# Kernel tuning notes

Hardware: AMD Instinct MI355X
Metric: run time of the kernel (lower is better)

The kernel has to match this reference:

```python
import jax, jax.numpy as jnp
import numpy as np

D_MODEL = 384
D_INNER = 768   # expand=2
D_STATE = 16
DT_RANK = 24    # ceil(d_model/16)
D_CONV = 4
VOCAB = 50257
AUDIO_DIM = 80
B, L_AUDIO, L_TEXT = 2, 1024, 1024


def _conv1d(x, w, b, pad_l, pad_r, groups=1):
    # x: [B, C, L], w: [O, I/groups, K]
    y = jax.lax.conv_general_dilated(
        x, w, window_strides=(1,), padding=[(pad_l, pad_r)],
        feature_group_count=groups, dimension_numbers=('NCH', 'OIH', 'NCH'))
    return y + b[None, :, None]


def _mamba(x, in_w, convw, convb, xproj_w, dt_w, dt_b, A_log, Dp, out_w):
    # x: [B, L, D_MODEL]
    Bn, L, _ = x.shape
    xz = x @ in_w.T                       # [B, L, 2*D_INNER]
    xi, z = jnp.split(xz, 2, axis=-1)
    # causal depthwise conv (torch pads d_conv-1 both sides then slices [:L])
    xi = _conv1d(xi.transpose(0, 2, 1), convw, convb, D_CONV - 1, 0, groups=D_INNER)
    xi = jax.nn.silu(xi.transpose(0, 2, 1))          # [B, L, D_INNER]
    xdbl = xi @ xproj_w.T                            # [B, L, DT_RANK+2*D_STATE]
    dt, Bm, Cm = jnp.split(xdbl, [DT_RANK, DT_RANK + D_STATE], axis=-1)
    dt = jax.nn.softplus(dt @ dt_w.T + dt_b)         # [B, L, D_INNER]
    A = -jnp.exp(A_log)                              # [D_INNER, D_STATE]
    dA = jnp.exp(dt[..., None] * A)                  # [B, L, D_INNER, D_STATE]
    dBu = dt[..., None] * Bm[:, :, None, :] * xi[..., None]

    def step(h, inputs):
        dA_t, dBu_t, C_t = inputs
        h = dA_t * h + dBu_t                         # [B, D_INNER, D_STATE]
        y = jnp.einsum('bdn,bn->bd', h, C_t)
        return h, y

    h0 = jnp.zeros((Bn, D_INNER, D_STATE), dtype=x.dtype)
    _, ys = jax.lax.scan(step, h0,
                         (dA.transpose(1, 0, 2, 3), dBu.transpose(1, 0, 2, 3), Cm.transpose(1, 0, 2)))
    y = ys.transpose(1, 0, 2) + xi * Dp              # D skip connection
    y = y * jax.nn.silu(z)                           # gate
    return y @ out_w.T                               # [B, L, D_MODEL]


def setup_inputs() -> dict:
    key = jax.random.key(0)
    ks = jax.random.split(key, 16)

    def rn(k, shape, s=0.02):
        return jax.random.normal(k, shape, jnp.float32) * s

    inp = {}
    inp['audio_features'] = jax.random.normal(ks[0], (B, AUDIO_DIM, L_AUDIO), jnp.float32)
    inp['text_tokens'] = jax.random.randint(ks[1], (B, L_TEXT), 0, VOCAB)
    inp['conv1_w'] = rn(ks[2], (D_MODEL // 2, AUDIO_DIM, 3))
    inp['conv1_b'] = jnp.zeros((D_MODEL // 2,), jnp.float32)
    inp['conv2_w'] = rn(ks[3], (D_MODEL, D_MODEL // 2, 3))
    inp['conv2_b'] = jnp.zeros((D_MODEL,), jnp.float32)
    inp['embed'] = rn(ks[4], (VOCAB, D_MODEL))

    def mamba_params(kbase):
        kk = jax.random.split(kbase, 6)
        A = jnp.tile(jnp.arange(1, D_STATE + 1, dtype=jnp.float32), (D_INNER, 1))
        return dict(in_w=rn(kk[0], (2 * D_INNER, D_MODEL)),
                    convw=rn(kk[1], (D_INNER, 1, D_CONV)),
                    convb=jnp.zeros((D_INNER,), jnp.float32),
                    xproj_w=rn(kk[2], (DT_RANK + 2 * D_STATE, D_INNER)),
                    dt_w=rn(kk[3], (D_INNER, DT_RANK)),
                    dt_b=rn(kk[4], (D_INNER,), 0.1),
                    A_log=jnp.log(A),
                    Dp=jnp.ones((D_INNER,), jnp.float32),
                    out_w=rn(kk[5], (D_MODEL, D_INNER)))

    for i, p in enumerate([mamba_params(ks[5]), mamba_params(ks[6])], 1):
        for n, v in p.items():
            inp[f'm{i}_{n}'] = v
    inp['proj_w'] = rn(ks[7], (VOCAB, D_MODEL))
    inp['proj_b'] = jnp.zeros((VOCAB,), jnp.float32)
    return inp


def reference(audio_features, text_tokens, conv1_w, conv1_b, conv2_w, conv2_b, embed,
              m1_in_w, m1_convw, m1_convb, m1_xproj_w, m1_dt_w, m1_dt_b, m1_A_log, m1_Dp, m1_out_w,
              m2_in_w, m2_convw, m2_convb, m2_xproj_w, m2_dt_w, m2_dt_b, m2_A_log, m2_Dp, m2_out_w,
              proj_w, proj_b):
    a = jax.nn.relu(_conv1d(audio_features, conv1_w, conv1_b, 1, 1))
    a = _conv1d(a, conv2_w, conv2_b, 1, 1)
    audio_emb = a.transpose(0, 2, 1)                 # [B, L_audio, D_MODEL]
    text_emb = embed[text_tokens]                    # [B, L_text, D_MODEL]
    x = jnp.concatenate([audio_emb, text_emb], axis=1)
    x = _mamba(x, m1_in_w, m1_convw, m1_convb, m1_xproj_w, m1_dt_w, m1_dt_b, m1_A_log, m1_Dp, m1_out_w)
    x = _mamba(x, m2_in_w, m2_convw, m2_convb, m2_xproj_w, m2_dt_w, m2_dt_b, m2_A_log, m2_Dp, m2_out_w)
    return x @ proj_w.T + proj_b                     # [B, L, VOCAB]
```

## Files before the change

kernel.cpp:

```cpp
#include <hip/hip_runtime.h>

typedef unsigned short u16;
typedef __attribute__((ext_vector_type(4))) float f4;
typedef __attribute__((ext_vector_type(4))) float f32x4;
typedef __attribute__((ext_vector_type(8))) short short8;
typedef __attribute__((ext_vector_type(4))) unsigned short u16x4;

#define DEV static __device__ __forceinline__

DEV u16 f2bf(float f) {
  unsigned u = __float_as_uint(f);
  u += 0x7fffu + ((u >> 16) & 1u);
  return (u16)(u >> 16);
}
DEV float siluf(float z) { return z / (1.f + __expf(-z)); }

DEV void gload16(const u16* g, const u16* l) {
  __builtin_amdgcn_global_load_lds(
      (const __attribute__((address_space(1))) unsigned int*)(unsigned long long)g,
      (__attribute__((address_space(3))) unsigned int*)(unsigned int)(unsigned long long)l,
      16, 0, 0);
}

struct CvtArgs {
  const float* src[9];
  u16* dst[9];
  int bstart[10];
  int nq[9];
};

DEV void cvt_plain(const float* __restrict__ s, u16* __restrict__ d, int q, int nq) {
  if (q < nq) {
    f4 v = ((const f4*)s)[q];
    u16x4 o;
#pragma unroll
    for (int e = 0; e < 4; ++e) o[e] = f2bf(v[e]);
    ((u16x4*)d)[q] = o;
  }
}
DEV void cvt_pad(const float* __restrict__ s, u16* __restrict__ d, int q, int nq) {
  if (q < nq) {
    int e0 = q * 4, n = e0 >> 5, k = e0 & 31;
    u16x4 o;
#pragma unroll
    for (int e = 0; e < 4; ++e) {
      int kk = k + e;
      float v = (kk < 24) ? s[n * 24 + kk] : 0.f;
      o[e] = f2bf(v);
    }
    ((u16x4*)d)[q] = o;
  }
}

__global__ void k_cvtmulti(CvtArgs a) {
  int b = blockIdx.x;
  int i = 0;
#pragma unroll
  for (int j = 1; j < 9; ++j) i += (b >= a.bstart[j]);
#pragma unroll
  for (int j = 0; j < 9; ++j) {
    if (i == j) {
      int q = (b - a.bstart[j]) * 256 + threadIdx.x;
      if (j == 2 || j == 6) cvt_pad(a.src[j], a.dst[j], q, a.nq[j]);
      else                  cvt_plain(a.src[j], a.dst[j], q, a.nq[j]);
    }
  }
}

__global__ void k_wtrans(const float* __restrict__ in, float* __restrict__ out, int O, int I) {
  int n = O * I * 3;
  for (int g = blockIdx.x * blockDim.x + threadIdx.x; g < n; g += gridDim.x * blockDim.x) {
    int o = g / (I * 3);
    int rem = g - o * (I * 3);
    out[rem * O + o] = in[g];
  }
}

__global__ __launch_bounds__(192) void k_conv1(const float* __restrict__ audio,
    const float* __restrict__ w1t, const float* __restrict__ b1, float* __restrict__ a1t) {
  __shared__ float s[80][18];
  int bx = blockIdx.x;
  int b = bx >> 6, l0 = (bx & 63) << 4;
  int tid = threadIdx.x;
  for (int i = tid; i < 80 * 18; i += 192) {
    int ci = i / 18, dl = i - ci * 18;
    int l = l0 + dl - 1;
    s[ci][dl] = (l >= 0 && l < 1024) ? audio[(b * 80 + ci) * 1024 + l] : 0.f;
  }
  __syncthreads();
  int co = tid;
  float acc[16];
  float bias = b1[co];
#pragma unroll
  for (int i = 0; i < 16; ++i) acc[i] = bias;
  for (int ci = 0; ci < 80; ++ci) {
#pragma unroll
    for (int j = 0; j < 3; ++j) {
      float w = w1t[(ci * 3 + j) * 192 + co];
#pragma unroll
      for (int ls = 0; ls < 16; ++ls) acc[ls] = fmaf(s[ci][ls + j], w, acc[ls]);
    }
  }
#pragma unroll
  for (int ls = 0; ls < 16; ++ls) {
    float v = acc[ls] > 0.f ? acc[ls] : 0.f;
    a1t[(b * 1024 + l0 + ls) * 192 + co] = v;
  }
}

__global__ __launch_bounds__(384) void k_conv2b(const float* __restrict__ a1t,
    const float* __restrict__ w2t, const float* __restrict__ b2, u16* __restrict__ Xb) {
  __shared__ float s[10][192];
  int bx = blockIdx.x;
  int b = bx >> 7, l0 = (bx & 127) << 3;
  int tid = threadIdx.x;
  for (int i = tid; i < 10 * 192; i += 384) {
    int dl = i / 192, ci = i - dl * 192;
    int l = l0 + dl - 1;
    s[dl][ci] = (l >= 0 && l < 1024) ? a1t[(b * 1024 + l) * 192 + ci] : 0.f;
  }
  __syncthreads();
  int co = tid;
  float acc[8];
  float bias = b2[co];
#pragma unroll
  for (int i = 0; i < 8; ++i) acc[i] = bias;
  for (int ci = 0; ci < 192; ++ci) {
#pragma unroll
    for (int j = 0; j < 3; ++j) {
      float w = w2t[(ci * 3 + j) * 384 + co];
#pragma unroll
      for (int ls = 0; ls < 8; ++ls) acc[ls] = fmaf(s[ls + j][ci], w, acc[ls]);
    }
  }
#pragma unroll
  for (int ls = 0; ls < 8; ++ls)
    Xb[((size_t)(b * 2048 + l0 + ls)) * 384 + co] = f2bf(acc[ls]);
}

__global__ void k_embedb(const int* __restrict__ tok, const float* __restrict__ emb,
                         u16* __restrict__ Xb) {
  int gid = blockIdx.x * blockDim.x + threadIdx.x;
  if (gid >= 2 * 1024 * 96) return;
  int q = gid % 96;
  int rt = gid / 96;
  int b = rt >> 10, t = rt & 1023;
  int tk = tok[b * 1024 + t];
  f4 v = *(const f4*)(emb + (size_t)tk * 384 + q * 4);
  u16x4 o;
#pragma unroll
  for (int e = 0; e < 4; ++e) o[e] = f2bf(v[e]);
  *(u16x4*)(Xb + ((size_t)(b * 2048 + 1024 + t)) * 384 + q * 4) = o;
}

__global__ void k_dwconv2(const float* __restrict__ xz, const float* __restrict__ cw,
                          const float* __restrict__ cb, float* __restrict__ xif,
                          u16* __restrict__ xib) {
  int gid = blockIdx.x * blockDim.x + threadIdx.x;
  if (gid >= 4096 * 192) return;
  int d4 = gid % 192;
  int row = gid / 192;
  int b = row >> 11, l = row & 2047;
  int d = d4 * 4;
  f4 cw0 = *(const f4*)(cw + d * 4);
  f4 cw1 = *(const f4*)(cw + d * 4 + 4);
  f4 cw2 = *(const f4*)(cw + d * 4 + 8);
  f4 cw3 = *(const f4*)(cw + d * 4 + 12);
  f4 acc = *(const f4*)(cb + d);
#pragma unroll
  for (int j = 0; j < 4; ++j) {
    int lj = l - 3 + j;
    if (lj >= 0) {
      f4 v = *(const f4*)(xz + ((size_t)(b * 2048 + lj)) * 1536 + d);
      acc[0] = fmaf(v[0], cw0[j], acc[0]);
      acc[1] = fmaf(v[1], cw1[j], acc[1]);
      acc[2] = fmaf(v[2], cw2[j], acc[2]);
      acc[3] = fmaf(v[3], cw3[j], acc[3]);
    }
  }
  f4 o;
  u16x4 ob;
#pragma unroll
  for (int e = 0; e < 4; ++e) { o[e] = siluf(acc[e]); ob[e] = f2bf(o[e]); }
  *(f4*)(xif + (size_t)row * 768 + d) = o;
  *(u16x4*)(xib + (size_t)row * 768 + d) = ob;
}

template <int TILE, int BIAS, int ACT, int OUTB, int SWZ>
__global__ __launch_bounds__(256) void k_gemm2(
    const u16* __restrict__ A, int lda, const u16* __restrict__ W, int ldw,
    const float* __restrict__ bias, float* __restrict__ C, u16* __restrict__ Cb,
    int ldc, int M, int N, int K) {
  constexpr int MF = (TILE == 128) ? 4 : 2;
  constexpr int TB = TILE * 32;
  __shared__ u16 As[2][TB], Ws[2][TB];
  int bid = blockIdx.x;
  if (SWZ) {
    int nwg = gridDim.x;
    int q = nwg >> 3, r = nwg & 7;
    int xcd = bid & 7, li = bid >> 3;
    bid = (xcd < r ? xcd * (q + 1) : r * (q + 1) + (xcd - r) * q) + li;
  }
  int bm, bn;
  if (TILE == 128) { bm = (bid & 31) << 7; bn = (bid >> 5) << 7; }
  else             { bm = (bid & 63) << 6; bn = (bid >> 6) << 6; }
  int t = threadIdx.x, lane = t & 63, wave = t >> 6;
  int wm0, wn0;
  if (TILE == 128) { wm0 = (wave >> 1) << 6; wn0 = (wave & 1) << 6; }
  else             { wm0 = (wave >> 1) << 5; wn0 = (wave & 1) << 5; }
  int fr = lane & 15, fk = (lane >> 4) << 3;
  int r0 = t >> 2, sl = (t & 3) << 3;
  const u16* gA0 = A + (size_t)(bm + r0) * lda + sl;
  const u16* gA1 = gA0 + (size_t)64 * lda;
  int n0 = bn + r0;      if (n0 > N - 1) n0 = N - 1;
  int n1 = bn + r0 + 64; if (n1 > N - 1) n1 = N - 1;
  const u16* gW0 = W + (size_t)n0 * ldw + sl;
  const u16* gW1 = W + (size_t)n1 * ldw + sl;
  f32x4 acc[MF][MF] = {};
  int nk = K >> 5;
  auto stage = [&](int buf, int k0) {
    gload16(gA0 + k0, As[buf] + t * 8);
    gload16(gW0 + k0, Ws[buf] + t * 8);
    if (TILE == 128) {
      gload16(gA1 + k0, As[buf] + t * 8 + 2048);
      gload16(gW1 + k0, Ws[buf] + t * 8 + 2048);
    }
  };
  stage(0, 0);
  __syncthreads();
  for (int s = 0; s < nk; ++s) {
    int cur = s & 1;
    short8 af[MF], wf[MF];
#pragma unroll
    for (int mi = 0; mi < MF; ++mi) af[mi] = *(const short8*)&As[cur][(wm0 + mi * 16 + fr) * 32 + fk];
#pragma unroll
    for (int ni = 0; ni < MF; ++ni) wf[ni] = *(const short8*)&Ws[cur][(wn0 + ni * 16 + fr) * 32 + fk];
    if (s + 1 < nk) stage(cur ^ 1, (s + 1) << 5);
#pragma unroll
    for (int mi = 0; mi < MF; ++mi)
#pragma unroll
      for (int ni = 0; ni < MF; ++ni)
        acc[mi][ni] = __builtin_amdgcn_mfma_f32_16x16x32_bf16(af[mi], wf[ni], acc[mi][ni], 0, 0, 0);
    __syncthreads();
  }
  int frow = (lane >> 4) << 2;
#pragma unroll
  for (int ni = 0; ni < MF; ++ni) {
    int col = bn + wn0 + ni * 16 + fr;
    if (col < N) {
      float bv = BIAS ? bias[col] : 0.f;
#pragma unroll
      for (int mi = 0; mi < MF; ++mi) {
        int row = bm + wm0 + mi * 16 + frow;
#pragma unroll
        for (int rr = 0; rr < 4; ++rr) {
          float v = acc[mi][ni][rr] + bv;
          if (ACT == 1) v = (v > 20.f) ? v : log1pf(__expf(v));
          size_t o = (size_t)(row + rr) * ldc + col;
          if (OUTB == 0) C[o] = v;
          else if (OUTB == 1) Cb[o] = f2bf(v);
          else { C[o] = v; Cb[o] = f2bf(v); }
        }
      }
    }
  }
}

__global__ __launch_bounds__(256, 4) void k_gemmF(
    const u16* __restrict__ A, const u16* __restrict__ W,
    const float* __restrict__ bias, float* __restrict__ C,
    int ldc, int N) {
  __shared__ __align__(16) char smraw[40960];
  u16* As = (u16*)smraw;
  u16* Ws = (u16*)(smraw + 8192);
  float* Cs = (float*)smraw;
  int bid = blockIdx.x;
  {
    int nwg = gridDim.x;
    int q = nwg >> 3, r = nwg & 7;
    int xcd = bid & 7, li = bid >> 3;
    bid = (xcd < r ? xcd * (q + 1) : r * (q + 1) + (xcd - r) * q) + li;
  }
  int bm = (bid & 63) << 6;
  int bn = (bid >> 6) << 8;
  int t = threadIdx.x, lane = t & 63, wave = t >> 6;
  int wm0 = (wave >> 1) << 5;
  int wn0 = (wave & 1) << 7;
  int fr = lane & 15, hi = lane >> 4, fk = hi << 3;
  int r0 = t >> 2, sl = (t & 3) << 3;
  const u16* gA = A + (size_t)(bm + r0) * 384 + sl;
  int nrow[4];
#pragma unroll
  for (int i = 0; i < 4; ++i) {
    int gn = bn + r0 + i * 64;
    nrow[i] = (gn > N - 1) ? (N - 1) : gn;
  }
  const u16* gWs = W + sl;
  f32x4 acc[2][8] = {};
  auto stage = [&](int buf, int k0) {
    gload16(gA + k0, As + buf * 2048 + t * 8);
#pragma unroll
    for (int i = 0; i < 4; ++i)
      gload16(gWs + (size_t)nrow[i] * 384 + k0, Ws + buf * 8192 + t * 8 + i * 2048);
  };
  stage(0, 0);
  __syncthreads();
  for (int s = 0; s < 12; ++s) {
    int cur = s & 1;
    short8 af[2];
#pragma unroll
    for (int mi = 0; mi < 2; ++mi)
      af[mi] = *(const short8*)&As[cur * 2048 + (wm0 + mi * 16 + fr) * 32 + fk];
    if (s + 1 < 12) stage(cur ^ 1, (s + 1) << 5);
#pragma unroll
    for (int ni = 0; ni < 8; ++ni) {
      short8 wf = *(const short8*)&Ws[cur * 8192 + (wn0 + ni * 16 + fr) * 32 + fk];
#pragma unroll
      for (int mi = 0; mi < 2; ++mi)
        acc[mi][ni] = __builtin_amdgcn_mfma_f32_16x16x32_bf16(af[mi], wf, acc[mi][ni], 0, 0, 0);
    }
    __syncthreads();
  }
  int cq = (t & 63) << 2;
  int gcol0 = bn + cq;
  f4 bv4;
  if (gcol0 + 3 < N) bv4 = *(const f4*)&bias[gcol0];
  else {
#pragma unroll
    for (int e = 0; e < 4; ++e) bv4[e] = (gcol0 + e < N) ? bias[gcol0 + e] : 0.f;
  }
  int frow = hi << 2;
#pragma unroll
  for (int c = 0; c < 2; ++c) {
    if (c) __syncthreads();
    if (wm0 == c * 32) {
#pragma unroll
      for (int ni = 0; ni < 8; ++ni) {
        int lc = wn0 + ni * 16 + fr;
#pragma unroll
        for (int mi = 0; mi < 2; ++mi)
#pragma unroll
          for (int rr = 0; rr < 4; ++rr)
            Cs[(mi * 16 + frow + rr) * 260 + lc] = acc[mi][ni][rr];
      }
    }
    __syncthreads();
#pragma unroll
    for (int p = 0; p < 8; ++p) {
      int lr = (p << 2) + (t >> 6);
      f4 v = *(const f4*)&Cs[lr * 260 + cq];
      v += bv4;
      float* cp = C + (size_t)(bm + c * 32 + lr) * ldc + gcol0;
      if (gcol0 + 3 < N) {
        __builtin_nontemporal_store(v, (f4*)cp);
      } else {
#pragma unroll
        for (int e = 0; e < 4; ++e)
          if (gcol0 + e < N) __builtin_nontemporal_store(v[e], cp + e);
      }
    }
  }
}

DEV int scan_ch0(int bx) { return (((bx & 7) * 24) + (bx >> 3)) * 4; }

__global__ __launch_bounds__(64) void k_scanA(
    const float* __restrict__ dt, const float* __restrict__ xdbl,
    const float* __restrict__ xi, const float* __restrict__ A_log,
    float* __restrict__ Hloc, float* __restrict__ Sdt) {
  int b = blockIdx.y, seg = blockIdx.z;
  int ch0 = scan_ch0(blockIdx.x);
  int tid = threadIdx.x;
  int c = tid >> 4, n = tid & 15;
  int d = ch0 + c;
  float a = -__expf(A_log[d * 16 + n]);
  float h = 0.f, sdt = 0.f;
  size_t row = (size_t)b * 2048 + seg * 64;
#pragma unroll 4
  for (int i = 0; i < 64; ++i, ++row) {
    float dtv = dt[row * 768 + d];
    float xiv = xi[row * 768 + d];
    float Bv = xdbl[row * 56 + 24 + n];
    float da = __expf(dtv * a);
    h = fmaf(da, h, dtv * Bv * xiv);
    sdt += dtv;
  }
  size_t o = (((size_t)b * 32 + seg) * 768 + d) * 16 + n;
  Hloc[o] = h;
  if (n == 0) Sdt[((size_t)b * 32 + seg) * 768 + d] = sdt;
}

__global__ __launch_bounds__(256) void k_scanB(
    const float* __restrict__ Hloc, const float* __restrict__ Sdt,
    const float* __restrict__ A_log, float* __restrict__ Hini) {
  int gid = blockIdx.x * 256 + threadIdx.x;
  if (gid >= 24576) return;
  int b = gid / 12288;
  int r = gid - b * 12288;
  int d = r >> 4, n = r & 15;
  float a = -__expf(A_log[d * 16 + n]);
  float h = 0.f;
  for (int s = 0; s < 32; ++s) {
    size_t o = (((size_t)b * 32 + s) * 768 + d) * 16 + n;
    Hini[o] = h;
    float P = __expf(a * Sdt[((size_t)b * 32 + s) * 768 + d]);
    h = fmaf(P, h, Hloc[o]);
  }
}

__global__ __launch_bounds__(64) void k_scanC(
    const float* __restrict__ dt, const float* __restrict__ xdbl,
    const float* __restrict__ xi, const float* __restrict__ xz,
    const float* __restrict__ A_log, const float* __restrict__ Dp,
    const float* __restrict__ Hini, u16* __restrict__ y) {
  __shared__ float s_y[64][4];
  int b = blockIdx.y, seg = blockIdx.z;
  int ch0 = scan_ch0(blockIdx.x);
  int tid = threadIdx.x;
  int c = tid >> 4, n = tid & 15;
  int d = ch0 + c;
  float a = -__expf(A_log[d * 16 + n]);
  float h = Hini[(((size_t)b * 32 + seg) * 768 + d) * 16 + n];
  size_t row = (size_t)b * 2048 + seg * 64;
#pragma unroll 2
  for (int i = 0; i < 64; ++i, ++row) {
    float dtv = dt[row * 768 + d];
    float xiv = xi[row * 768 + d];
    float Bv = xdbl[row * 56 + 24 + n];
    float Cv = xdbl[row * 56 + 40 + n];
    float da = __expf(dtv * a);
    h = fmaf(da, h, dtv * Bv * xiv);
    float yv = h * Cv;
    yv += __shfl_xor(yv, 1);
    yv += __shfl_xor(yv, 2);
    yv += __shfl_xor(yv, 4);
    yv += __shfl_xor(yv, 8);
    if (n == 0) s_y[i][c] = yv;
  }
  __syncthreads();
  size_t rw = (size_t)b * 2048 + seg * 64 + tid;
  f4 xiv4 = *(const f4*)(xi + rw * 768 + ch0);
  f4 dpv = *(const f4*)(Dp + ch0);
  f4 zv = *(const f4*)(xz + rw * 1536 + 768 + ch0);
  u16x4 ob;
#pragma unroll
  for (int e = 0; e < 4; ++e) {
    float o = (s_y[tid][e] + xiv4[e] * dpv[e]) * siluf(zv[e]);
    ob[e] = f2bf(o);
  }
  *(u16x4*)(y + rw * 768 + ch0) = ob;
}

extern "C" void kernel_launch(void* const* d_in, const int* in_sizes, int n_in,
                              void* d_out, int out_size, void* d_ws, size_t ws_size,
                              hipStream_t stream) {
  const float* audio   = (const float*)d_in[0];
  const int*   tokens  = (const int*)d_in[1];
  const float* conv1_w = (const float*)d_in[2];
  const float* conv1_b = (const float*)d_in[3];
  const float* conv2_w = (const float*)d_in[4];
  const float* conv2_b = (const float*)d_in[5];
  const float* embedw  = (const float*)d_in[6];
  const float* P1[9], *P2[9];
  for (int i = 0; i < 9; ++i) { P1[i] = (const float*)d_in[7 + i]; P2[i] = (const float*)d_in[16 + i]; }
  const float* proj_w = (const float*)d_in[25];
  const float* proj_b = (const float*)d_in[26];
  (void)in_sizes; (void)n_in; (void)out_size; (void)ws_size;

  float* base = (float*)d_out;
  size_t off = 0;
  auto af = [&](size_t n) { float* p = base + off; off += n; return p; };
  float* xz   = af((size_t)4096 * 1536);
  float* xif  = af((size_t)4096 * 768);
  float* xdbl = af((size_t)4096 * 56);
  float* dtb  = af((size_t)4096 * 768);
  float* a1t  = af((size_t)2 * 1024 * 192);
  float* w1t  = af((size_t)80 * 3 * 192);
  float* w2t  = af((size_t)192 * 3 * 384);
  float* Hloc = af((size_t)2 * 32 * 768 * 16);
  float* Hini = af((size_t)2 * 32 * 768 * 16);
  float* Sdt  = af((size_t)2 * 32 * 768);
  u16* ub = (u16*)(base + off);
  size_t uoff = 0;
  auto au = [&](size_t n) { u16* p = ub + uoff; uoff += n; return p; };
  u16* Xin_b  = au((size_t)4096 * 384);
  u16* Xmid_b = au((size_t)4096 * 384);
  u16* xib    = au((size_t)4096 * 768);
  u16* xdblb  = au((size_t)4096 * 56);
  u16* yb16   = au((size_t)4096 * 768);
  u16* Wi1 = au((size_t)1536 * 384);
  u16* Wx1 = au((size_t)56 * 768);
  u16* Wd1 = au((size_t)768 * 32);
  u16* Wo1 = au((size_t)384 * 768);
  u16* Wi2 = au((size_t)1536 * 384);
  u16* Wx2 = au((size_t)56 * 768);
  u16* Wd2 = au((size_t)768 * 32);
  u16* Wo2 = au((size_t)384 * 768);
  u16* X2b    = (u16*)d_ws;
  u16* projwb = X2b + (size_t)4096 * 384;

  CvtArgs ca;
  const float* srcs[9] = {P1[0], P1[3], P1[4], P1[8], P2[0], P2[3], P2[4], P2[8], proj_w};
  u16* dsts[9] = {Wi1, Wx1, Wd1, Wo1, Wi2, Wx2, Wd2, Wo2, projwb};
  int nqs[9] = {147456, 10752, 6144, 73728, 147456, 10752, 6144, 73728, 4824672};
  int cum = 0;
  for (int j = 0; j < 9; ++j) {
    ca.src[j] = srcs[j]; ca.dst[j] = dsts[j]; ca.nq[j] = nqs[j];
    ca.bstart[j] = cum; cum += (nqs[j] + 255) / 256;
  }
  ca.bstart[9] = cum;
  k_cvtmulti<<<dim3(cum), dim3(256), 0, stream>>>(ca);

  k_wtrans<<<dim3(180), dim3(256), 0, stream>>>(conv1_w, w1t, 192, 80);
  k_wtrans<<<dim3(864), dim3(256), 0, stream>>>(conv2_w, w2t, 384, 192);
  k_conv1<<<dim3(128), dim3(192), 0, stream>>>(audio, w1t, conv1_b, a1t);
  k_conv2b<<<dim3(256), dim3(384), 0, stream>>>(a1t, w2t, conv2_b, Xin_b);
  k_embedb<<<dim3(768), dim3(256), 0, stream>>>(tokens, embedw, Xin_b);

  auto run_mamba = [&](const float* const* P, const u16* Xin, u16* Xout,
                       const u16* Wi, const u16* Wx, const u16* Wd, const u16* Wo) {
    k_gemm2<64, 0, 0, 0, 1><<<dim3(64 * 24), dim3(256), 0, stream>>>(
        Xin, 384, Wi, 384, nullptr, xz, nullptr, 1536, 4096, 1536, 384);
    k_dwconv2<<<dim3(3072), dim3(256), 0, stream>>>(xz, P[1], P[2], xif, xib);
    k_gemm2<64, 0, 0, 2, 0><<<dim3(64 * 1), dim3(256), 0, stream>>>(
        xib, 768, Wx, 768, nullptr, xdbl, xdblb, 56, 4096, 56, 768);
    k_gemm2<64, 1, 1, 0, 0><<<dim3(64 * 12), dim3(256), 0, stream>>>(
        xdblb, 56, Wd, 32, P[5], dtb, nullptr, 768, 4096, 768, 32);
    k_scanA<<<dim3(192, 2, 32), dim3(64), 0, stream>>>(dtb, xdbl, xif, P[6], Hloc, Sdt);
    k_scanB<<<dim3(96), dim3(256), 0, stream>>>(Hloc, Sdt, P[6], Hini);
    k_scanC<<<dim3(192, 2, 32), dim3(64), 0, stream>>>(dtb, xdbl, xif, xz, P[6], P[7], Hini, yb16);
    k_gemm2<64, 0, 0, 1, 0><<<dim3(64 * 6), dim3(256), 0, stream>>>(
        yb16, 768, Wo, 768, nullptr, nullptr, Xout, 384, 4096, 384, 768);
  };
  run_mamba(P1, Xin_b, Xmid_b, Wi1, Wx1, Wd1, Wo1);
  run_mamba(P2, Xmid_b, X2b, Wi2, Wx2, Wd2, Wo2);

  k_gemmF<<<dim3(64 * 197), dim3(256), 0, stream>>>(
      X2b, projwb, proj_b, (float*)d_out, 50257, 50257);
}
```

Before: 648.2 us.

## Fuse dt projection and inter-segment carry into scan kernels, regroup final GEMM tiles

```diff
diff --git a/kernel.cpp b/kernel.cpp
--- a/kernel.cpp
+++ b/kernel.cpp
@@ -23,10 +23,10 @@
 }
 
 struct CvtArgs {
-  const float* src[9];
-  u16* dst[9];
-  int bstart[10];
-  int nq[9];
+  const float* src[7];
+  u16* dst[7];
+  int bstart[8];
+  int nq[7];
 };
 
 DEV void cvt_plain(const float* __restrict__ s, u16* __restrict__ d, int q, int nq) {
@@ -38,32 +38,16 @@
     ((u16x4*)d)[q] = o;
   }
 }
-DEV void cvt_pad(const float* __restrict__ s, u16* __restrict__ d, int q, int nq) {
-  if (q < nq) {
-    int e0 = q * 4, n = e0 >> 5, k = e0 & 31;
-    u16x4 o;
-#pragma unroll
-    for (int e = 0; e < 4; ++e) {
-      int kk = k + e;
-      float v = (kk < 24) ? s[n * 24 + kk] : 0.f;
-      o[e] = f2bf(v);
-    }
-    ((u16x4*)d)[q] = o;
-  }
-}
 
 __global__ void k_cvtmulti(CvtArgs a) {
   int b = blockIdx.x;
   int i = 0;
 #pragma unroll
-  for (int j = 1; j < 9; ++j) i += (b >= a.bstart[j]);
-#pragma unroll
-  for (int j = 0; j < 9; ++j) {
-    if (i == j) {
-      int q = (b - a.bstart[j]) * 256 + threadIdx.x;
-      if (j == 2 || j == 6) cvt_pad(a.src[j], a.dst[j], q, a.nq[j]);
-      else                  cvt_plain(a.src[j], a.dst[j], q, a.nq[j]);
-    }
+  for (int j = 1; j < 7; ++j) i += (b >= a.bstart[j]);
+#pragma unroll
+  for (int j = 0; j < 7; ++j) {
+    if (i == j)
+      cvt_plain(a.src[j], a.dst[j], (b - a.bstart[j]) * 256 + threadIdx.x, a.nq[j]);
   }
 }
 
@@ -281,8 +265,11 @@
     int xcd = bid & 7, li = bid >> 3;
     bid = (xcd < r ? xcd * (q + 1) : r * (q + 1) + (xcd - r) * q) + li;
   }
-  int bm = (bid & 63) << 6;
-  int bn = (bid >> 6) << 8;
+  int mg = bid / 1576;
+  int rem = bid - mg * 1576;
+  int np = rem >> 3, mi = rem & 7;
+  int bm = ((mg << 3) + mi) << 6;
+  int bn = np << 8;
   int t = threadIdx.x, lane = t & 63, wave = t >> 6;
   int wm0 = (wave >> 1) << 5;
   int wn0 = (wave & 1) << 7;
@@ -309,15 +296,15 @@
     int cur = s & 1;
     short8 af[2];
 #pragma unroll
-    for (int mi = 0; mi < 2; ++mi)
-      af[mi] = *(const short8*)&As[cur * 2048 + (wm0 + mi * 16 + fr) * 32 + fk];
+    for (int mi2 = 0; mi2 < 2; ++mi2)
+      af[mi2] = *(const short8*)&As[cur * 2048 + (wm0 + mi2 * 16 + fr) * 32 + fk];
     if (s + 1 < 12) stage(cur ^ 1, (s + 1) << 5);
 #pragma unroll
     for (int ni = 0; ni < 8; ++ni) {
       short8 wf = *(const short8*)&Ws[cur * 8192 + (wn0 + ni * 16 + fr) * 32 + fk];
 #pragma unroll
-      for (int mi = 0; mi < 2; ++mi)
-        acc[mi][ni] = __builtin_amdgcn_mfma_f32_16x16x32_bf16(af[mi], wf, acc[mi][ni], 0, 0, 0);
+      for (int mi2 = 0; mi2 < 2; ++mi2)
+        acc[mi2][ni] = __builtin_amdgcn_mfma_f32_16x16x32_bf16(af[mi2], wf, acc[mi2][ni], 0, 0, 0);
     }
     __syncthreads();
   }
@@ -338,10 +325,10 @@
       for (int ni = 0; ni < 8; ++ni) {
         int lc = wn0 + ni * 16 + fr;
 #pragma unroll
-        for (int mi = 0; mi < 2; ++mi)
+        for (int mi2 = 0; mi2 < 2; ++mi2)
 #pragma unroll
           for (int rr = 0; rr < 4; ++rr)
-            Cs[(mi * 16 + frow + rr) * 260 + lc] = acc[mi][ni][rr];
+            Cs[(mi2 * 16 + frow + rr) * 260 + lc] = acc[mi2][ni][rr];
       }
     }
     __syncthreads();
@@ -364,21 +351,55 @@
 
 DEV int scan_ch0(int bx) { return (((bx & 7) * 24) + (bx >> 3)) * 4; }
 
+DEV void dt_inline(const float* __restrict__ xdbl, size_t rowbase, int tid,
+                   const float* __restrict__ s_w, const float* __restrict__ s_b,
+                   float (*s_dt)[4]) {
+  const float* xr = xdbl + (rowbase + tid) * 56;
+  f4 x0 = *(const f4*)xr,        x1 = *(const f4*)(xr + 4),  x2 = *(const f4*)(xr + 8);
+  f4 x3 = *(const f4*)(xr + 12), x4 = *(const f4*)(xr + 16), x5 = *(const f4*)(xr + 20);
+#pragma unroll
+  for (int cc = 0; cc < 4; ++cc) {
+    const float* w = s_w + cc * 24;
+    float acc = s_b[cc];
+#pragma unroll
+    for (int q = 0; q < 4; ++q) acc = fmaf(x0[q], w[q], acc);
+#pragma unroll
+    for (int q = 0; q < 4; ++q) acc = fmaf(x1[q], w[4 + q], acc);
+#pragma unroll
+    for (int q = 0; q < 4; ++q) acc = fmaf(x2[q], w[8 + q], acc);
+#pragma unroll
+    for (int q = 0; q < 4; ++q) acc = fmaf(x3[q], w[12 + q], acc);
+#pragma unroll
+    for (int q = 0; q < 4; ++q) acc = fmaf(x4[q], w[16 + q], acc);
+#pragma unroll
+    for (int q = 0; q < 4; ++q) acc = fmaf(x5[q], w[20 + q], acc);
+    s_dt[tid][cc] = (acc > 20.f) ? acc : log1pf(__expf(acc));
+  }
+}
+
 __global__ __launch_bounds__(64) void k_scanA(
-    const float* __restrict__ dt, const float* __restrict__ xdbl,
-    const float* __restrict__ xi, const float* __restrict__ A_log,
+    const float* __restrict__ xdbl, const float* __restrict__ xi,
+    const float* __restrict__ A_log,
+    const float* __restrict__ dtw, const float* __restrict__ dtbias,
     float* __restrict__ Hloc, float* __restrict__ Sdt) {
+  __shared__ float s_dt[64][4], s_w[96], s_b[4];
   int b = blockIdx.y, seg = blockIdx.z;
   int ch0 = scan_ch0(blockIdx.x);
   int tid = threadIdx.x;
   int c = tid >> 4, n = tid & 15;
   int d = ch0 + c;
+  for (int i = tid; i < 96; i += 64) s_w[i] = dtw[ch0 * 24 + i];
+  if (tid < 4) s_b[tid] = dtbias[ch0 + tid];
+  size_t rowbase = (size_t)b * 2048 + seg * 64;
+  __syncthreads();
+  dt_inline(xdbl, rowbase, tid, s_w, s_b, s_dt);
+  __syncthreads();
   float a = -__expf(A_log[d * 16 + n]);
   float h = 0.f, sdt = 0.f;
-  size_t row = (size_t)b * 2048 + seg * 64;
+  size_t row = rowbase;
 #pragma unroll 4
   for (int i = 0; i < 64; ++i, ++row) {
-    float dtv = dt[row * 768 + d];
+    float dtv = s_dt[i][c];
     float xiv = xi[row * 768 + d];
     float Bv = xdbl[row * 56 + 24 + n];
     float da = __expf(dtv * a);
@@ -390,41 +411,35 @@
   if (n == 0) Sdt[((size_t)b * 32 + seg) * 768 + d] = sdt;
 }
 
-__global__ __launch_bounds__(256) void k_scanB(
+__global__ __launch_bounds__(64) void k_scanC(
+    const float* __restrict__ xdbl, const float* __restrict__ xi,
+    const float* __restrict__ xz, const float* __restrict__ A_log,
+    const float* __restrict__ Dp,
+    const float* __restrict__ dtw, const float* __restrict__ dtbias,
     const float* __restrict__ Hloc, const float* __restrict__ Sdt,
-    const float* __restrict__ A_log, float* __restrict__ Hini) {
-  int gid = blockIdx.x * 256 + threadIdx.x;
-  if (gid >= 24576) return;
-  int b = gid / 12288;
-  int r = gid - b * 12288;
-  int d = r >> 4, n = r & 15;
-  float a = -__expf(A_log[d * 16 + n]);
-  float h = 0.f;
-  for (int s = 0; s < 32; ++s) {
-    size_t o = (((size_t)b * 32 + s) * 768 + d) * 16 + n;
-    Hini[o] = h;
-    float P = __expf(a * Sdt[((size_t)b * 32 + s) * 768 + d]);
-    h = fmaf(P, h, Hloc[o]);
-  }
-}
-
-__global__ __launch_bounds__(64) void k_scanC(
-    const float* __restrict__ dt, const float* __restrict__ xdbl,
-    const float* __restrict__ xi, const float* __restrict__ xz,
-    const float* __restrict__ A_log, const float* __restrict__ Dp,
-    const float* __restrict__ Hini, u16* __restrict__ y) {
-  __shared__ float s_y[64][4];
+    u16* __restrict__ y) {
+  __shared__ float s_dt[64][4], s_y[64][4], s_w[96], s_b[4];
   int b = blockIdx.y, seg = blockIdx.z;
   int ch0 = scan_ch0(blockIdx.x);
   int tid = threadIdx.x;
   int c = tid >> 4, n = tid & 15;
   int d = ch0 + c;
+  for (int i = tid; i < 96; i += 64) s_w[i] = dtw[ch0 * 24 + i];
+  if (tid < 4) s_b[tid] = dtbias[ch0 + tid];
+  size_t rowbase = (size_t)b * 2048 + seg * 64;
+  __syncthreads();
+  dt_inline(xdbl, rowbase, tid, s_w, s_b, s_dt);
   float a = -__expf(A_log[d * 16 + n]);
-  float h = Hini[(((size_t)b * 32 + seg) * 768 + d) * 16 + n];
-  size_t row = (size_t)b * 2048 + seg * 64;
+  float h = 0.f;
+  for (int s = 0; s < seg; ++s) {
+    float P = __expf(a * Sdt[((size_t)b * 32 + s) * 768 + d]);
+    h = fmaf(P, h, Hloc[(((size_t)b * 32 + s) * 768 + d) * 16 + n]);
+  }
+  __syncthreads();
+  size_t row = rowbase;
 #pragma unroll 2
   for (int i = 0; i < 64; ++i, ++row) {
-    float dtv = dt[row * 768 + d];
+    float dtv = s_dt[i][c];
     float xiv = xi[row * 768 + d];
     float Bv = xdbl[row * 56 + 24 + n];
     float Cv = xdbl[row * 56 + 40 + n];
@@ -438,7 +453,7 @@
     if (n == 0) s_y[i][c] = yv;
   }
   __syncthreads();
-  size_t rw = (size_t)b * 2048 + seg * 64 + tid;
+  size_t rw = rowbase + tid;
   f4 xiv4 = *(const f4*)(xi + rw * 768 + ch0);
   f4 dpv = *(const f4*)(Dp + ch0);
   f4 zv = *(const f4*)(xz + rw * 1536 + 768 + ch0);
@@ -473,12 +488,10 @@
   float* xz   = af((size_t)4096 * 1536);
   float* xif  = af((size_t)4096 * 768);
   float* xdbl = af((size_t)4096 * 56);
-  float* dtb  = af((size_t)4096 * 768);
   float* a1t  = af((size_t)2 * 1024 * 192);
   float* w1t  = af((size_t)80 * 3 * 192);
   float* w2t  = af((size_t)192 * 3 * 384);
   float* Hloc = af((size_t)2 * 32 * 768 * 16);
-  float* Hini = af((size_t)2 * 32 * 768 * 16);
   float* Sdt  = af((size_t)2 * 32 * 768);
   u16* ub = (u16*)(base + off);
   size_t uoff = 0;
@@ -486,29 +499,26 @@
   u16* Xin_b  = au((size_t)4096 * 384);
   u16* Xmid_b = au((size_t)4096 * 384);
   u16* xib    = au((size_t)4096 * 768);
-  u16* xdblb  = au((size_t)4096 * 56);
   u16* yb16   = au((size_t)4096 * 768);
   u16* Wi1 = au((size_t)1536 * 384);
   u16* Wx1 = au((size_t)56 * 768);
-  u16* Wd1 = au((size_t)768 * 32);
   u16* Wo1 = au((size_t)384 * 768);
   u16* Wi2 = au((size_t)1536 * 384);
   u16* Wx2 = au((size_t)56 * 768);
-  u16* Wd2 = au((size_t)768 * 32);
   u16* Wo2 = au((size_t)384 * 768);
   u16* X2b    = (u16*)d_ws;
   u16* projwb = X2b + (size_t)4096 * 384;
 
   CvtArgs ca;
-  const float* srcs[9] = {P1[0], P1[3], P1[4], P1[8], P2[0], P2[3], P2[4], P2[8], proj_w};
-  u16* dsts[9] = {Wi1, Wx1, Wd1, Wo1, Wi2, Wx2, Wd2, Wo2, projwb};
-  int nqs[9] = {147456, 10752, 6144, 73728, 147456, 10752, 6144, 73728, 4824672};
+  const float* srcs[7] = {P1[0], P1[3], P1[8], P2[0], P2[3], P2[8], proj_w};
+  u16* dsts[7] = {Wi1, Wx1, Wo1, Wi2, Wx2, Wo2, projwb};
+  int nqs[7] = {147456, 10752, 73728, 147456, 10752, 73728, 4824672};
   int cum = 0;
-  for (int j = 0; j < 9; ++j) {
+  for (int j = 0; j < 7; ++j) {
     ca.src[j] = srcs[j]; ca.dst[j] = dsts[j]; ca.nq[j] = nqs[j];
     ca.bstart[j] = cum; cum += (nqs[j] + 255) / 256;
   }
-  ca.bstart[9] = cum;
+  ca.bstart[7] = cum;
   k_cvtmulti<<<dim3(cum), dim3(256), 0, stream>>>(ca);
 
   k_wtrans<<<dim3(180), dim3(256), 0, stream>>>(conv1_w, w1t, 192, 80);
@@ -518,22 +528,21 @@
   k_embedb<<<dim3(768), dim3(256), 0, stream>>>(tokens, embedw, Xin_b);
 
   auto run_mamba = [&](const float* const* P, const u16* Xin, u16* Xout,
-                       const u16* Wi, const u16* Wx, const u16* Wd, const u16* Wo) {
+                       const u16* Wi, const u16* Wx, const u16* Wo) {
     k_gemm2<64, 0, 0, 0, 1><<<dim3(64 * 24), dim3(256), 0, stream>>>(
         Xin, 384, Wi, 384, nullptr, xz, nullptr, 1536, 4096, 1536, 384);
     k_dwconv2<<<dim3(3072), dim3(256), 0, stream>>>(xz, P[1], P[2], xif, xib);
-    k_gemm2<64, 0, 0, 2, 0><<<dim3(64 * 1), dim3(256), 0, stream>>>(
-        xib, 768, Wx, 768, nullptr, xdbl, xdblb, 56, 4096, 56, 768);
-    k_gemm2<64, 1, 1, 0, 0><<<dim3(64 * 12), dim3(256), 0, stream>>>(
-        xdblb, 56, Wd, 32, P[5], dtb, nullptr, 768, 4096, 768, 32);
-    k_scanA<<<dim3(192, 2, 32), dim3(64), 0, stream>>>(dtb, xdbl, xif, P[6], Hloc, Sdt);
-    k_scanB<<<dim3(96), dim3(256), 0, stream>>>(Hloc, Sdt, P[6], Hini);
-    k_scanC<<<dim3(192, 2, 32), dim3(64), 0, stream>>>(dtb, xdbl, xif, xz, P[6], P[7], Hini, yb16);
+    k_gemm2<64, 0, 0, 0, 0><<<dim3(64 * 1), dim3(256), 0, stream>>>(
+        xib, 768, Wx, 768, nullptr, xdbl, nullptr, 56, 4096, 56, 768);
+    k_scanA<<<dim3(192, 2, 32), dim3(64), 0, stream>>>(
+        xdbl, xif, P[6], P[4], P[5], Hloc, Sdt);
+    k_scanC<<<dim3(192, 2, 32), dim3(64), 0, stream>>>(
+        xdbl, xif, xz, P[6], P[7], P[4], P[5], Hloc, Sdt, yb16);
     k_gemm2<64, 0, 0, 1, 0><<<dim3(64 * 6), dim3(256), 0, stream>>>(
         yb16, 768, Wo, 768, nullptr, nullptr, Xout, 384, 4096, 384, 768);
   };
-  run_mamba(P1, Xin_b, Xmid_b, Wi1, Wx1, Wd1, Wo1);
-  run_mamba(P2, Xmid_b, X2b, Wi2, Wx2, Wd2, Wo2);
+  run_mamba(P1, Xin_b, Xmid_b, Wi1, Wx1, Wo1);
+  run_mamba(P2, Xmid_b, X2b, Wi2, Wx2, Wo2);
 
   k_gemmF<<<dim3(64 * 197), dim3(256), 0, stream>>>(
       X2b, projwb, proj_b, (float*)d_out, 50257, 50257);
```

New measurement: 633.0 us. 2.3% less time.
